# Kernel tuning notes

Hardware: AMD Instinct MI355X
Metric: run time of the kernel (lower is better)

Reference implementation:

```python
import jax, jax.numpy as jnp
import numpy as np

N = 10000       # num_nodes
E = 1000        # num_hyperedges
STEPS = 30      # horizon


def setup_inputs() -> dict:
    key = jax.random.key(0)
    k1, k2 = jax.random.split(key, 2)
    infected0 = jax.random.uniform(k1, (N,)) < 0.01
    x = jnp.stack([(~infected0).astype(jnp.float32),
                   infected0.astype(jnp.float32),
                   jnp.zeros((N,), jnp.float32)], axis=1)
    H = (jax.random.uniform(k2, (STEPS - 1, E, N)) < 0.001).astype(jnp.float32)
    beta = jnp.full((N,), 0.01, jnp.float32)
    gamma = jnp.full((N,), 0.038, jnp.float32)
    return {"x": x, "H": H, "beta": beta, "gamma": gamma, "steps": STEPS}


def _simulate(x, H, beta, gamma):
    n = x.shape[0]
    key0 = jax.random.key(42)

    def step(carry, H_t):
        p_prev, s_prev, key = carry
        key, k1, k2 = jax.random.split(key, 3)
        infected = s_prev[:, 1]
        # hypergraph Laplacian step: H_t.T @ (H_t @ infected)
        new_cases = beta * (H_t.T @ (H_t @ infected))
        new_rec = gamma * infected
        p = jnp.stack([p_prev[:, 0] - new_cases,
                       p_prev[:, 1] + new_cases - new_rec,
                       p_prev[:, 2] + new_rec], axis=1)
        p = jnp.clip(p, 0.0, 1.0)
        # per-node stochastic SIR state transitions (vectorized)
        u1 = jax.random.uniform(k1, (n,))
        u2 = jax.random.uniform(k2, (n,))
        was_S = s_prev[:, 0] == 1
        was_I = s_prev[:, 1] == 1
        s_to_I = was_S & (u1 < p[:, 1])
        i_event = was_I & (u1 < p[:, 2])
        i_to_R = i_event & (u2 < 0.5)
        i_to_S = i_event & ~(u2 < 0.5)
        new_S = (was_S & ~s_to_I) | i_to_S
        new_I = s_to_I | (was_I & ~i_event)
        new_R = (~was_S & ~was_I) | i_to_R
        s = jnp.stack([new_S, new_I, new_R], axis=1).astype(x.dtype)
        return (p, s, key), (p, s)

    (_, _, _), (p_seq, s_seq) = jax.lax.scan(step, (x, x, key0), H)
    pathogen = jnp.concatenate([x[None], p_seq], axis=0)    # (steps, N, 3)
    state = jnp.concatenate([x[None], s_seq], axis=0)       # (steps, N, 3)
    return pathogen, state


def reference(x, H, beta, gamma, steps):
    # steps == H.shape[0] + 1 by construction
    return _simulate(x, H, beta, gamma)
```

## Files before the change

### kernel.cpp

```cpp
#include <hip/hip_runtime.h>
#include <stdint.h>

constexpr int NN = 10000;
constexpr int EE = 1000;
constexpr int TT = 30;
constexpr int TS = TT - 1;
constexpr int ROW = NN * 3;
constexpr int S_OFF = TT * ROW;
constexpr int CAP_E = 48;
constexpr int WPR = CAP_E / 2;
constexpr int PREW = 8;
constexpr int SIMT = 1024;
constexpr int NPT  = 10;
constexpr int NROWS = TS * EE;
constexpr int F4R   = NN / 4;
constexpr int RPB   = 20;
constexpr int PK    = 5;
constexpr int SCANB = NROWS / RPB;
constexpr unsigned GATE = EE + 1;
static_assert(EE % RPB == 0 && NROWS % RPB == 0 && RPB % PK == 0, "geometry");

__host__ __device__ inline void tf2x32(uint32_t k0, uint32_t k1,
                                       uint32_t x0, uint32_t x1,
                                       uint32_t &o0, uint32_t &o1) {
  uint32_t ks2 = k0 ^ k1 ^ 0x1BD11BDAu;
  x0 += k0; x1 += k1;
#define TFR(r) do { x0 += x1; x1 = (x1 << (r)) | (x1 >> (32 - (r))); x1 ^= x0; } while (0)
  TFR(13); TFR(15); TFR(26); TFR(6);
  x0 += k1;  x1 += ks2 + 1u;
  TFR(17); TFR(29); TFR(16); TFR(24);
  x0 += ks2; x1 += k0 + 2u;
  TFR(13); TFR(15); TFR(26); TFR(6);
  x0 += k0;  x1 += k1 + 3u;
  TFR(17); TFR(29); TFR(16); TFR(24);
  x0 += k1;  x1 += ks2 + 4u;
  TFR(13); TFR(15); TFR(26); TFR(6);
  x0 += ks2; x1 += k0 + 5u;
#undef TFR
  o0 = x0; o1 = x1;
}

__device__ inline float bits_to_uniform(uint32_t bits) {
  float f = __uint_as_float((bits >> 9) | 0x3F800000u) - 1.0f;
  return f < 0.f ? 0.f : f;
}

struct StepKeys { uint32_t k1a[TS], k1b[TS], k2a[TS], k2b[TS]; };

__device__ inline void bar_lds() {
  asm volatile("s_waitcnt lgkmcnt(0)\n\ts_barrier" ::: "memory");
}

#define ALD(p)     __hip_atomic_load((p),  __ATOMIC_RELAXED, __HIP_MEMORY_SCOPE_AGENT)
#define AST(p, v)  __hip_atomic_store((p), (v), __ATOMIC_RELAXED, __HIP_MEMORY_SCOPE_AGENT)

__global__ void k_zero(unsigned* __restrict__ cnt) {
  if (threadIdx.x < TS) cnt[threadIdx.x] = 0u;
}

__global__ __launch_bounds__(SIMT, 4)
void k_fused(const float* __restrict__ H,
             int* __restrict__ edge_cnt, uint32_t* __restrict__ edge_words,
             unsigned long long* __restrict__ uv, unsigned* __restrict__ cntg,
             const float* __restrict__ x,
             const float* __restrict__ beta, const float* __restrict__ gamma_,
             float* __restrict__ out, StepKeys keys) {
  const int tid = threadIdx.x;
  const int bi  = blockIdx.x;

  if (bi >= 1 && bi <= TS) {
    const int t = bi - 1;
#pragma unroll
    for (int k = 0; k < NPT; ++k) {
      int n = tid + k * SIMT;
      if (n < NN) {
        uint32_t a, b;
        tf2x32(keys.k1a[t], keys.k1b[t], 0u, (uint32_t)n, a, b);
        uint32_t b1 = __float_as_uint(bits_to_uniform(a ^ b));
        tf2x32(keys.k2a[t], keys.k2b[t], 0u, (uint32_t)n, a, b);
        uint32_t b2 = __float_as_uint(bits_to_uniform(a ^ b));
        unsigned long long raw = (unsigned long long)b1 | ((unsigned long long)b2 << 32);
        AST(&uv[(size_t)t * NN + n], raw);
      }
    }
    __syncthreads();
    if (tid == 0)
      __hip_atomic_fetch_add(&cntg[t], 1u, __ATOMIC_RELAXED, __HIP_MEMORY_SCOPE_AGENT);
    return;
  }

  if (bi > TS) {
    const int base = (bi - 1 - TS) * RPB;
    const int t    = base / EE;
    const int e0   = base - t * EE;

    __shared__ int      scnt_arr[RPB];
    __shared__ uint16_t lists[RPB][CAP_E];
    if (tid < RPB) scnt_arr[tid] = 0;

    const float4* h0 = reinterpret_cast<const float4*>(H) + (size_t)base * F4R;
    const bool has2 = tid < F4R - 2048;

    float4 b0[PK], b1[PK], b2[PK];
#pragma unroll
    for (int p = 0; p < PK; ++p) {
      const float4* hr = h0 + (size_t)p * F4R;
      b0[p] = hr[tid];
      b1[p] = hr[tid + 1024];
      b2[p] = has2 ? hr[tid + 2048] : make_float4(0.f, 0.f, 0.f, 0.f);
    }
    bar_lds();

#define PROCS(vv, b4, rr) do { \
    if ((vv).x != 0.f) { int q = atomicAdd(&scnt_arr[rr], 1); if (q < CAP_E) lists[rr][q] = (uint16_t)((b4) + 0); } \
    if ((vv).y != 0.f) { int q = atomicAdd(&scnt_arr[rr], 1); if (q < CAP_E) lists[rr][q] = (uint16_t)((b4) + 1); } \
    if ((vv).z != 0.f) { int q = atomicAdd(&scnt_arr[rr], 1); if (q < CAP_E) lists[rr][q] = (uint16_t)((b4) + 2); } \
    if ((vv).w != 0.f) { int q = atomicAdd(&scnt_arr[rr], 1); if (q < CAP_E) lists[rr][q] = (uint16_t)((b4) + 3); } \
  } while (0)

    for (int o = 0; o < RPB / PK; ++o) {
#pragma unroll
      for (int p = 0; p < PK; ++p) {
        const int r = o * PK + p;
        float4 va = b0[p], vb = b1[p], vc = b2[p];
        if (o + 1 < RPB / PK) {
          const float4* hr = h0 + (size_t)(r + PK) * F4R;
          b0[p] = hr[tid];
          b1[p] = hr[tid + 1024];
          if (has2) b2[p] = hr[tid + 2048];
        }
        PROCS(va, 4 * tid, r);
        PROCS(vb, 4 * (tid + 1024), r);
        if (has2) PROCS(vc, 4 * (tid + 2048), r);
        bar_lds();
        int c = scnt_arr[r]; c = c < CAP_E ? c : CAP_E;
        const int row = base + r, e = e0 + r;
        if (tid == 0) AST(&edge_cnt[row], c);
        int words = (c + 1) >> 1;
        int wmax = words > PREW ? words : PREW;
        if (tid < wmax) {
          uint32_t lo = (2 * tid     < c) ? (uint32_t)lists[r][2 * tid]     : 0xFFFFu;
          uint32_t hi = (2 * tid + 1 < c) ? (uint32_t)lists[r][2 * tid + 1] : 0xFFFFu;
          AST(&edge_words[((size_t)t * WPR + tid) * EE + e], lo | (hi << 16));
        }
      }
    }
#undef PROCS
    __syncthreads();
    if (tid == 0)
      __hip_atomic_fetch_add(&cntg[t], (unsigned)RPB,
                             __ATOMIC_RELAXED, __HIP_MEMORY_SCOPE_AGENT);
    return;
  }

  __shared__ int nvst[NN];
  __shared__ unsigned char st8[NN];

  float p0a[NPT], p1a[NPT], p2a[NPT], bet[NPT], gam[NPT], u1r[NPT], u2r[NPT];
#pragma unroll
  for (int k = 0; k < NPT; ++k) {
    int n = tid + k * SIMT;
    if (n < NN) {
      float x0 = x[n * 3 + 0], x1 = x[n * 3 + 1], x2 = x[n * 3 + 2];
      p0a[k] = x0; p1a[k] = x1; p2a[k] = x2;
      st8[n] = (unsigned char)((x1 == 1.f) ? 1 : ((x0 == 1.f) ? 0 : 2));
      nvst[n] = 0;
      bet[k] = beta[n]; gam[k] = gamma_[n];
      out[n * 3 + 0] = x0; out[n * 3 + 1] = x1; out[n * 3 + 2] = x2;
      out[S_OFF + n * 3 + 0] = x0; out[S_OFF + n * 3 + 1] = x1; out[S_OFF + n * 3 + 2] = x2;
    }
  }
  bar_lds();

  if (tid == 0) {
    while (ALD(&cntg[0]) < GATE) __builtin_amdgcn_s_sleep(1);
  }
  bar_lds();
  int ec = 0; uint32_t w[PREW];
  if (tid < EE) {
    ec = ALD(&edge_cnt[tid]); if (ec > CAP_E) ec = CAP_E;
#pragma unroll
    for (int j = 0; j < PREW; ++j) w[j] = ALD(&edge_words[(size_t)j * EE + tid]);
  }
#pragma unroll
  for (int k = 0; k < NPT; ++k) {
    int n = tid + k * SIMT;
    if (n < NN) {
      unsigned long long raw = ALD(&uv[n]);
      u1r[k] = __uint_as_float((uint32_t)raw);
      u2r[k] = __uint_as_float((uint32_t)(raw >> 32));
    }
  }

  for (int t = 0; t < TS; ++t) {
    if (tid < EE) {
      const uint32_t* wb = edge_words + (size_t)t * WPR * EE + tid;
      int words = (ec + 1) >> 1;
      int s = 0;
#pragma unroll
      for (int j = 0; j < PREW; ++j) {
        uint32_t lo = w[j] & 0xFFFFu, hi = w[j] >> 16;
        if (lo != 0xFFFFu) s += (st8[lo] == 1) ? 1 : 0;
        if (hi != 0xFFFFu) s += (st8[hi] == 1) ? 1 : 0;
      }
      for (int j = PREW; j < words; ++j) {
        uint32_t ww = ALD(&wb[(size_t)j * EE]);
        uint32_t lo = ww & 0xFFFFu, hi = ww >> 16;
        if (lo != 0xFFFFu) s += (st8[lo] == 1) ? 1 : 0;
        if (hi != 0xFFFFu) s += (st8[hi] == 1) ? 1 : 0;
      }
      if (s > 0) {
#pragma unroll
        for (int j = 0; j < PREW; ++j) {
          uint32_t lo = w[j] & 0xFFFFu, hi = w[j] >> 16;
          if (lo != 0xFFFFu) atomicAdd(&nvst[lo], s);
          if (hi != 0xFFFFu) atomicAdd(&nvst[hi], s);
        }
        for (int j = PREW; j < words; ++j) {
          uint32_t ww = ALD(&wb[(size_t)j * EE]);
          uint32_t lo = ww & 0xFFFFu, hi = ww >> 16;
          if (lo != 0xFFFFu) atomicAdd(&nvst[lo], s);
          if (hi != 0xFFFFu) atomicAdd(&nvst[hi], s);
        }
      }
    }
    bar_lds();

    const bool more = (t + 1 < TS);
    if (more && tid == 0) {
      while (ALD(&cntg[t + 1]) < GATE) __builtin_amdgcn_s_sleep(1);
    }
    bar_lds();
    int ecn = 0; uint32_t wn[PREW];
    if (more && tid < EE) {
      ecn = ALD(&edge_cnt[(t + 1) * EE + tid]); if (ecn > CAP_E) ecn = CAP_E;
#pragma unroll
      for (int j = 0; j < PREW; ++j)
        wn[j] = ALD(&edge_words[((size_t)(t + 1) * WPR + j) * EE + tid]);
    }

    float* po = out + (size_t)(t + 1) * ROW;
    float* so = out + S_OFF + (size_t)(t + 1) * ROW;
#pragma unroll
    for (int k = 0; k < NPT; ++k) {
      int n = tid + k * SIMT;
      if (n < NN) {
        int v  = nvst[n];
        int st = (int)st8[n];
        float s1 = (st == 1) ? 1.f : 0.f;
        float new_cases = __fmul_rn(bet[k], (float)v);
        float new_rec   = __fmul_rn(gam[k], s1);
        float q0 = fminf(1.f, fmaxf(0.f, __fsub_rn(p0a[k], new_cases)));
        float q1 = fminf(1.f, fmaxf(0.f, __fsub_rn(__fadd_rn(p1a[k], new_cases), new_rec)));
        float q2 = fminf(1.f, fmaxf(0.f, __fadd_rn(p2a[k], new_rec)));
        p0a[k] = q0; p1a[k] = q1; p2a[k] = q2;

        bool was_S  = (st == 0);
        bool was_I  = (st == 1);
        bool s_to_I = was_S && (u1r[k] < q1);
        bool i_event = was_I && (u1r[k] < q2);
        bool u2lt   = (u2r[k] < 0.5f);
        bool i_to_R = i_event && u2lt;
        bool i_to_S = i_event && !u2lt;
        bool new_S = (was_S && !s_to_I) || i_to_S;
        bool new_I = s_to_I || (was_I && !i_event);
        bool new_R = (!was_S && !was_I) || i_to_R;

        po[n * 3 + 0] = q0; po[n * 3 + 1] = q1; po[n * 3 + 2] = q2;
        so[n * 3 + 0] = new_S ? 1.f : 0.f;
        so[n * 3 + 1] = new_I ? 1.f : 0.f;
        so[n * 3 + 2] = new_R ? 1.f : 0.f;
        st8[n] = (unsigned char)(new_I ? 1 : (new_S ? 0 : 2));
        nvst[n] = 0;
      }
    }

    if (more) {
#pragma unroll
      for (int k = 0; k < NPT; ++k) {
        int n = tid + k * SIMT;
        if (n < NN) {
          unsigned long long raw = ALD(&uv[(size_t)(t + 1) * NN + n]);
          u1r[k] = __uint_as_float((uint32_t)raw);
          u2r[k] = __uint_as_float((uint32_t)(raw >> 32));
        }
      }
      ec = ecn;
#pragma unroll
      for (int j = 0; j < PREW; ++j) w[j] = wn[j];
    }
    bar_lds();
  }
}

extern "C" void kernel_launch(void* const* d_in, const int* in_sizes, int n_in,
                              void* d_out, int out_size, void* d_ws, size_t ws_size,
                              hipStream_t stream) {
  const float* x      = (const float*)d_in[0];
  const float* H      = (const float*)d_in[1];
  const float* beta   = (const float*)d_in[2];
  const float* gamma_ = (const float*)d_in[3];
  float* out = (float*)d_out;

  StepKeys keys;
  uint32_t key0 = 0u, key1 = 42u;
  for (int t = 0; t < TS; ++t) {
    uint32_t a0, b0, a1, b1, a2, b2;
    tf2x32(key0, key1, 0u, 0u, a0, b0);
    tf2x32(key0, key1, 0u, 1u, a1, b1);
    tf2x32(key0, key1, 0u, 2u, a2, b2);
    keys.k1a[t] = a1; keys.k1b[t] = b1; keys.k2a[t] = a2; keys.k2b[t] = b2;
    key0 = a0; key1 = b0;
  }

  size_t off = 0;
  auto take = [&](size_t bytes) { size_t o = off; off += (bytes + 255) & ~(size_t)255; return o; };
  size_t o_ec = take((size_t)NROWS * sizeof(int));
  size_t o_ew = take((size_t)TS * WPR * EE * sizeof(uint32_t));
  size_t o_uv = take((size_t)TS * NN * sizeof(unsigned long long));
  size_t o_ct = take((size_t)TS * sizeof(unsigned));

  int*      edge_cnt   = (int*)((char*)d_ws + o_ec);
  uint32_t* edge_words = (uint32_t*)((char*)d_ws + o_ew);
  unsigned long long* uvp = (unsigned long long*)((char*)d_ws + o_uv);
  unsigned* cnt        = (unsigned*)((char*)d_ws + o_ct);

  k_zero<<<1, 64, 0, stream>>>(cnt);
  k_fused<<<1 + TS + SCANB, SIMT, 0, stream>>>(H, edge_cnt, edge_words, uvp, cnt,
                                               x, beta, gamma_, out, keys);
}
```

Before: 1.693 ms.

## Split sequential simulation across four blocks exchanging per-step state via global memory

The serial SIR time-stepping, once run by a single block, is now split across four blocks. Each block owns a quarter of the nodes' probability and update work plus the output writes. Each block still gathers over all hyperedges but only scatters into its own slice, then publishes its state bytes to a global buffer and spins until all four blocks have published before reloading the full state. This is meant to cut per-block node work and output-store bandwidth on the critical path. The cost is a cross-block global barrier every step and redundant edge gathering in every block.

```diff
diff --git a/kernel.cpp b/kernel.cpp
--- a/kernel.cpp
+++ b/kernel.cpp
@@ -12,6 +12,11 @@
 constexpr int PREW = 8;
 constexpr int SIMT = 1024;
 constexpr int NPT  = 10;
+constexpr int SIMW = 4;
+constexpr int SLICE = NN / SIMW;
+constexpr int SNPT = (SLICE + SIMT - 1) / SIMT;
+constexpr int STQ  = NN / 4;
+constexpr int QW   = SLICE / 4;
 constexpr int NROWS = TS * EE;
 constexpr int F4R   = NN / 4;
 constexpr int RPB   = 20;
@@ -54,22 +59,23 @@
 #define ALD(p)     __hip_atomic_load((p),  __ATOMIC_RELAXED, __HIP_MEMORY_SCOPE_AGENT)
 #define AST(p, v)  __hip_atomic_store((p), (v), __ATOMIC_RELAXED, __HIP_MEMORY_SCOPE_AGENT)
 
-__global__ void k_zero(unsigned* __restrict__ cnt) {
-  if (threadIdx.x < TS) cnt[threadIdx.x] = 0u;
+__global__ void k_zero(unsigned* __restrict__ cnt, unsigned* __restrict__ scnt) {
+  if (threadIdx.x < TS) { cnt[threadIdx.x] = 0u; scnt[threadIdx.x] = 0u; }
 }
 
 __global__ __launch_bounds__(SIMT, 4)
 void k_fused(const float* __restrict__ H,
              int* __restrict__ edge_cnt, uint32_t* __restrict__ edge_words,
              unsigned long long* __restrict__ uv, unsigned* __restrict__ cntg,
+             unsigned* __restrict__ stbuf, unsigned* __restrict__ scnt,
              const float* __restrict__ x,
              const float* __restrict__ beta, const float* __restrict__ gamma_,
              float* __restrict__ out, StepKeys keys) {
   const int tid = threadIdx.x;
   const int bi  = blockIdx.x;
 
-  if (bi >= 1 && bi <= TS) {
-    const int t = bi - 1;
+  if (bi >= SIMW && bi < SIMW + TS) {
+    const int t = bi - SIMW;
 #pragma unroll
     for (int k = 0; k < NPT; ++k) {
       int n = tid + k * SIMT;
@@ -89,8 +95,8 @@
     return;
   }
 
-  if (bi > TS) {
-    const int base = (bi - 1 - TS) * RPB;
+  if (bi >= SIMW + TS) {
+    const int base = (bi - SIMW - TS) * RPB;
     const int t    = base / EE;
     const int e0   = base - t * EE;
 
@@ -153,24 +159,34 @@
     return;
   }
 
-  __shared__ int nvst[NN];
-  __shared__ unsigned char st8[NN];
-
-  float p0a[NPT], p1a[NPT], p2a[NPT], bet[NPT], gam[NPT], u1r[NPT], u2r[NPT];
+  const int bs   = bi;
+  const int base = bs * SLICE;
+  __shared__ unsigned st8w[STQ];
+  __shared__ int      nv[SLICE];
+  unsigned char* st8 = (unsigned char*)st8w;
+
 #pragma unroll
   for (int k = 0; k < NPT; ++k) {
     int n = tid + k * SIMT;
     if (n < NN) {
+      float x0 = x[n * 3 + 0], x1 = x[n * 3 + 1];
+      st8[n] = (unsigned char)((x1 == 1.f) ? 1 : ((x0 == 1.f) ? 0 : 2));
+    }
+  }
+  float p0a[SNPT], p1a[SNPT], p2a[SNPT], bet[SNPT], gam[SNPT], u1r[SNPT], u2r[SNPT];
+#pragma unroll
+  for (int k = 0; k < SNPT; ++k) {
+    int nl = tid + k * SIMT;
+    if (nl < SLICE) {
+      int n = base + nl;
       float x0 = x[n * 3 + 0], x1 = x[n * 3 + 1], x2 = x[n * 3 + 2];
       p0a[k] = x0; p1a[k] = x1; p2a[k] = x2;
-      st8[n] = (unsigned char)((x1 == 1.f) ? 1 : ((x0 == 1.f) ? 0 : 2));
-      nvst[n] = 0;
       bet[k] = beta[n]; gam[k] = gamma_[n];
       out[n * 3 + 0] = x0; out[n * 3 + 1] = x1; out[n * 3 + 2] = x2;
       out[S_OFF + n * 3 + 0] = x0; out[S_OFF + n * 3 + 1] = x1; out[S_OFF + n * 3 + 2] = x2;
     }
   }
-  bar_lds();
+  for (int i = tid; i < SLICE; i += SIMT) nv[i] = 0;
 
   if (tid == 0) {
     while (ALD(&cntg[0]) < GATE) __builtin_amdgcn_s_sleep(1);
@@ -183,10 +199,10 @@
     for (int j = 0; j < PREW; ++j) w[j] = ALD(&edge_words[(size_t)j * EE + tid]);
   }
 #pragma unroll
-  for (int k = 0; k < NPT; ++k) {
-    int n = tid + k * SIMT;
-    if (n < NN) {
-      unsigned long long raw = ALD(&uv[n]);
+  for (int k = 0; k < SNPT; ++k) {
+    int nl = tid + k * SIMT;
+    if (nl < SLICE) {
+      unsigned long long raw = ALD(&uv[base + nl]);
       u1r[k] = __uint_as_float((uint32_t)raw);
       u2r[k] = __uint_as_float((uint32_t)(raw >> 32));
     }
@@ -212,40 +228,28 @@
       if (s > 0) {
 #pragma unroll
         for (int j = 0; j < PREW; ++j) {
-          uint32_t lo = w[j] & 0xFFFFu, hi = w[j] >> 16;
-          if (lo != 0xFFFFu) atomicAdd(&nvst[lo], s);
-          if (hi != 0xFFFFu) atomicAdd(&nvst[hi], s);
+          unsigned r0 = (w[j] & 0xFFFFu) - (unsigned)base;
+          unsigned r1 = (w[j] >> 16) - (unsigned)base;
+          if (r0 < (unsigned)SLICE) atomicAdd(&nv[r0], s);
+          if (r1 < (unsigned)SLICE) atomicAdd(&nv[r1], s);
         }
         for (int j = PREW; j < words; ++j) {
           uint32_t ww = ALD(&wb[(size_t)j * EE]);
-          uint32_t lo = ww & 0xFFFFu, hi = ww >> 16;
-          if (lo != 0xFFFFu) atomicAdd(&nvst[lo], s);
-          if (hi != 0xFFFFu) atomicAdd(&nvst[hi], s);
+          unsigned r0 = (ww & 0xFFFFu) - (unsigned)base;
+          unsigned r1 = (ww >> 16) - (unsigned)base;
+          if (r0 < (unsigned)SLICE) atomicAdd(&nv[r0], s);
+          if (r1 < (unsigned)SLICE) atomicAdd(&nv[r1], s);
         }
       }
     }
     bar_lds();
 
-    const bool more = (t + 1 < TS);
-    if (more && tid == 0) {
-      while (ALD(&cntg[t + 1]) < GATE) __builtin_amdgcn_s_sleep(1);
-    }
-    bar_lds();
-    int ecn = 0; uint32_t wn[PREW];
-    if (more && tid < EE) {
-      ecn = ALD(&edge_cnt[(t + 1) * EE + tid]); if (ecn > CAP_E) ecn = CAP_E;
-#pragma unroll
-      for (int j = 0; j < PREW; ++j)
-        wn[j] = ALD(&edge_words[((size_t)(t + 1) * WPR + j) * EE + tid]);
-    }
-
-    float* po = out + (size_t)(t + 1) * ROW;
-    float* so = out + S_OFF + (size_t)(t + 1) * ROW;
-#pragma unroll
-    for (int k = 0; k < NPT; ++k) {
-      int n = tid + k * SIMT;
-      if (n < NN) {
-        int v  = nvst[n];
+#pragma unroll
+    for (int k = 0; k < SNPT; ++k) {
+      int nl = tid + k * SIMT;
+      if (nl < SLICE) {
+        int n  = base + nl;
+        int v  = nv[nl];
         int st = (int)st8[n];
         float s1 = (st == 1) ? 1.f : 0.f;
         float new_cases = __fmul_rn(bet[k], (float)v);
@@ -260,36 +264,68 @@
         bool s_to_I = was_S && (u1r[k] < q1);
         bool i_event = was_I && (u1r[k] < q2);
         bool u2lt   = (u2r[k] < 0.5f);
-        bool i_to_R = i_event && u2lt;
         bool i_to_S = i_event && !u2lt;
         bool new_S = (was_S && !s_to_I) || i_to_S;
         bool new_I = s_to_I || (was_I && !i_event);
-        bool new_R = (!was_S && !was_I) || i_to_R;
-
-        po[n * 3 + 0] = q0; po[n * 3 + 1] = q1; po[n * 3 + 2] = q2;
-        so[n * 3 + 0] = new_S ? 1.f : 0.f;
-        so[n * 3 + 1] = new_I ? 1.f : 0.f;
-        so[n * 3 + 2] = new_R ? 1.f : 0.f;
         st8[n] = (unsigned char)(new_I ? 1 : (new_S ? 0 : 2));
-        nvst[n] = 0;
-      }
-    }
-
+        nv[nl] = 0;
+      }
+    }
+    bar_lds();
+
+    if (tid < QW) AST(&stbuf[(size_t)t * STQ + bs * QW + tid], st8w[bs * QW + tid]);
+    __syncthreads();
+    if (tid == 0)
+      __hip_atomic_fetch_add(&scnt[t], 1u, __ATOMIC_RELAXED, __HIP_MEMORY_SCOPE_AGENT);
+
+    float* po = out + (size_t)(t + 1) * ROW;
+    float* so = out + S_OFF + (size_t)(t + 1) * ROW;
+#pragma unroll
+    for (int k = 0; k < SNPT; ++k) {
+      int nl = tid + k * SIMT;
+      if (nl < SLICE) {
+        int n = base + nl;
+        po[n * 3 + 0] = p0a[k]; po[n * 3 + 1] = p1a[k]; po[n * 3 + 2] = p2a[k];
+        int stn = (int)st8[n];
+        so[n * 3 + 0] = (stn == 0) ? 1.f : 0.f;
+        so[n * 3 + 1] = (stn == 1) ? 1.f : 0.f;
+        so[n * 3 + 2] = (stn == 2) ? 1.f : 0.f;
+      }
+    }
+
+    const bool more = (t + 1 < TS);
     if (more) {
-#pragma unroll
-      for (int k = 0; k < NPT; ++k) {
-        int n = tid + k * SIMT;
-        if (n < NN) {
-          unsigned long long raw = ALD(&uv[(size_t)(t + 1) * NN + n]);
+      if (tid == 0) {
+        while (ALD(&cntg[t + 1]) < GATE) __builtin_amdgcn_s_sleep(1);
+      }
+      bar_lds();
+      int ecn = 0; uint32_t wn[PREW];
+      if (tid < EE) {
+        ecn = ALD(&edge_cnt[(t + 1) * EE + tid]); if (ecn > CAP_E) ecn = CAP_E;
+#pragma unroll
+        for (int j = 0; j < PREW; ++j)
+          wn[j] = ALD(&edge_words[((size_t)(t + 1) * WPR + j) * EE + tid]);
+      }
+#pragma unroll
+      for (int k = 0; k < SNPT; ++k) {
+        int nl = tid + k * SIMT;
+        if (nl < SLICE) {
+          unsigned long long raw = ALD(&uv[(size_t)(t + 1) * NN + base + nl]);
           u1r[k] = __uint_as_float((uint32_t)raw);
           u2r[k] = __uint_as_float((uint32_t)(raw >> 32));
         }
       }
+      if (tid == 0) {
+        while (ALD(&scnt[t]) < (unsigned)SIMW) __builtin_amdgcn_s_sleep(1);
+      }
+      bar_lds();
+      for (int i = tid; i < STQ; i += SIMT)
+        st8w[i] = ALD(&stbuf[(size_t)t * STQ + i]);
+      bar_lds();
       ec = ecn;
 #pragma unroll
       for (int j = 0; j < PREW; ++j) w[j] = wn[j];
     }
-    bar_lds();
   }
 }
 
@@ -318,14 +354,18 @@
   size_t o_ec = take((size_t)NROWS * sizeof(int));
   size_t o_ew = take((size_t)TS * WPR * EE * sizeof(uint32_t));
   size_t o_uv = take((size_t)TS * NN * sizeof(unsigned long long));
+  size_t o_sb = take((size_t)TS * STQ * sizeof(unsigned));
   size_t o_ct = take((size_t)TS * sizeof(unsigned));
+  size_t o_sc = take((size_t)TS * sizeof(unsigned));
 
   int*      edge_cnt   = (int*)((char*)d_ws + o_ec);
   uint32_t* edge_words = (uint32_t*)((char*)d_ws + o_ew);
   unsigned long long* uvp = (unsigned long long*)((char*)d_ws + o_uv);
+  unsigned* stbuf      = (unsigned*)((char*)d_ws + o_sb);
   unsigned* cnt        = (unsigned*)((char*)d_ws + o_ct);
-
-  k_zero<<<1, 64, 0, stream>>>(cnt);
-  k_fused<<<1 + TS + SCANB, SIMT, 0, stream>>>(H, edge_cnt, edge_words, uvp, cnt,
-                                               x, beta, gamma_, out, keys);
-}
+  unsigned* scn        = (unsigned*)((char*)d_ws + o_sc);
+
+  k_zero<<<1, 64, 0, stream>>>(cnt, scn);
+  k_fused<<<SIMW + TS + SCANB, SIMT, 0, stream>>>(H, edge_cnt, edge_words, uvp, cnt,
+                                                  stbuf, scn, x, beta, gamma_, out, keys);
+}
```

Result: faster. 1.533 ms (-9.4%).
